# Kernel optimization log

Hardware: AMD Instinct MI355X
Metric: run time of the kernel (lower is better)

Reference implementation:

```python
import jax, jax.numpy as jnp
import numpy as np

B, C, H, W = 32, 4, 512, 512


def setup_inputs() -> dict:
    key = jax.random.key(0)
    k1, k2 = jax.random.split(key)
    out = jax.random.normal(k1, (B, C, H, W), dtype=jnp.float32)
    true_masks = jax.random.randint(k2, (B, H, W), 0, C, dtype=jnp.int32)
    return {"true_masks": true_masks, "out": out}


def reference(true_masks, out):
    n_classes = out.shape[1]
    # argmax over the class dim == torch's permute+reshape+max(dim=1)
    pred = jnp.argmax(out, axis=1).reshape(-1)          # [B*H*W]
    true = true_masks.reshape(-1)                        # [B*H*W]
    # single-pass histogram counts for all classes (replaces per-class loop)
    tp = jnp.bincount(pred, weights=(pred == true).astype(jnp.float32),
                      length=n_classes)                  # [C]
    pred_cnt = jnp.bincount(pred, length=n_classes).astype(jnp.float32)
    true_cnt = jnp.bincount(true, length=n_classes).astype(jnp.float32)
    dice = 2.0 * tp / (pred_cnt + true_cnt)              # [C]
    return dice[1:]                                      # skip background class 0
```

## Files before the change

### kernel.cpp

```cpp
#include <hip/hip_runtime.h>

constexpr int kHW       = 512 * 512;
constexpr int kC        = 4;
constexpr int kReplicas = 16;
constexpr int kLine     = 32;

constexpr int kWsInts = kReplicas * 12 * kLine;

__global__ __launch_bounds__(256)
void dice_count_kernel(const int* __restrict__ tm, const float* __restrict__ outp,
                       unsigned* __restrict__ cnt, int num_groups) {
    unsigned long long predp = 0, truep = 0, tpp = 0;

    const int stride = gridDim.x * blockDim.x;
    for (int g = blockIdx.x * blockDim.x + threadIdx.x; g < num_groups; g += stride) {
        const int b   = g >> 16;
        const int rem = (g & 0xFFFF) << 2;
        const float* base = outp + ((size_t)b * kC) * kHW + rem;
        const float4 v0 = *(const float4*)(base);
        const float4 v1 = *(const float4*)(base + kHW);
        const float4 v2 = *(const float4*)(base + 2 * kHW);
        const float4 v3 = *(const float4*)(base + 3 * kHW);
        const int4   t  = *(const int4*)(tm + (size_t)g * 4);

        #define DO_PIXEL(f, tf)                                        \
        {                                                              \
            int   pred = 0;                                            \
            float best = v0.f;                                         \
            if (v1.f > best) { best = v1.f; pred = 1; }                \
            if (v2.f > best) { best = v2.f; pred = 2; }                \
            if (v3.f > best) { best = v3.f; pred = 3; }                \
            predp += 1ull << (pred << 4);                              \
            truep += 1ull << (t.tf << 4);                              \
            if (pred == t.tf) tpp += 1ull << (pred << 4);              \
        }
        DO_PIXEL(x, x) DO_PIXEL(y, y) DO_PIXEL(z, z) DO_PIXEL(w, w)
        #undef DO_PIXEL
    }

    for (int off = 32; off > 0; off >>= 1) {
        predp += __shfl_down(predp, off);
        truep += __shfl_down(truep, off);
        tpp   += __shfl_down(tpp, off);
    }

    __shared__ unsigned long long s[3][4];
    const int lane = threadIdx.x & 63;
    const int wave = threadIdx.x >> 6;
    if (lane == 0) { s[0][wave] = predp; s[1][wave] = truep; s[2][wave] = tpp; }
    __syncthreads();

    if (threadIdx.x == 0) {
        unsigned long long P = s[0][0] + s[0][1] + s[0][2] + s[0][3];
        unsigned long long T = s[1][0] + s[1][1] + s[1][2] + s[1][3];
        unsigned long long Q = s[2][0] + s[2][1] + s[2][2] + s[2][3];
        unsigned* rep = cnt + (blockIdx.x & (kReplicas - 1)) * 12 * kLine;
        #pragma unroll
        for (int c = 0; c < 4; ++c) {
            atomicAdd(&rep[c * kLine],       (unsigned)((P >> (c * 16)) & 0xFFFF));
            atomicAdd(&rep[(4 + c) * kLine], (unsigned)((T >> (c * 16)) & 0xFFFF));
            atomicAdd(&rep[(8 + c) * kLine], (unsigned)((Q >> (c * 16)) & 0xFFFF));
        }
    }
}

__global__ void dice_final_kernel(const unsigned* __restrict__ cnt,
                                  float* __restrict__ out) {
    __shared__ float tot[12];
    if (threadIdx.x < 12) {
        unsigned sum = 0;
        #pragma unroll
        for (int r = 0; r < kReplicas; ++r)
            sum += cnt[(r * 12 + (int)threadIdx.x) * kLine];
        tot[threadIdx.x] = (float)sum;
    }
    __syncthreads();
    if (threadIdx.x >= 1 && threadIdx.x < 4) {
        const int c = (int)threadIdx.x;
        out[c - 1] = 2.0f * tot[8 + c] / (tot[c] + tot[4 + c]);
    }
}

extern "C" void kernel_launch(void* const* d_in, const int* in_sizes, int n_in,
                              void* d_out, int out_size, void* d_ws, size_t ws_size,
                              hipStream_t stream) {
    const int*   tm = (const int*)d_in[0];
    const float* op = (const float*)d_in[1];
    unsigned*   cnt = (unsigned*)d_ws;

    const int P = in_sizes[0];
    const int num_groups = P / 4;

    hipMemsetAsync(cnt, 0, kWsInts * sizeof(unsigned), stream);

    dice_count_kernel<<<1024, 256, 0, stream>>>(tm, op, cnt, num_groups);
    dice_final_kernel<<<1, 64, 0, stream>>>(cnt, (float*)d_out);
}
```

Before: 213.5 us.

## Replace atomics and memset with per-block partials and compile-time unrolled loop

Each block now writes its packed per-class partial counts to its own workspace slot instead of doing atomic adds into replicated counters. That removes the memset launch and the atomic contention. The grid doubles to 2048 blocks and the grid-stride loop becomes a fully unrolled loop with a fixed trip count, so more loads can be in flight. The final kernel reduces 2048 partials with 256 threads and shuffles. Problem sizes are now hard-coded at compile time, so the kernel no longer uses the runtime input size.

```diff
diff --git a/kernel.cpp b/kernel.cpp
--- a/kernel.cpp
+++ b/kernel.cpp
@@ -1,19 +1,25 @@
 #include <hip/hip_runtime.h>
 
-constexpr int kHW       = 512 * 512;
-constexpr int kC        = 4;
-constexpr int kReplicas = 16;
-constexpr int kLine     = 32;
+constexpr int kHW      = 512 * 512;
+constexpr int kC       = 4;
+constexpr int kB       = 32;
+constexpr int kGroups  = kB * kHW / 4;
+constexpr int kBlocks  = 2048;
+constexpr int kThreads = 256;
+constexpr int kStride  = kBlocks * kThreads;
+constexpr int kIters   = kGroups / kStride;
+static_assert(kGroups % kStride == 0, "grid must tile the group count exactly");
 
-constexpr int kWsInts = kReplicas * 12 * kLine;
 
-__global__ __launch_bounds__(256)
+__global__ __launch_bounds__(kThreads)
 void dice_count_kernel(const int* __restrict__ tm, const float* __restrict__ outp,
-                       unsigned* __restrict__ cnt, int num_groups) {
+                       unsigned long long* __restrict__ part) {
     unsigned long long predp = 0, truep = 0, tpp = 0;
+    const int tid0 = blockIdx.x * kThreads + threadIdx.x;
 
-    const int stride = gridDim.x * blockDim.x;
-    for (int g = blockIdx.x * blockDim.x + threadIdx.x; g < num_groups; g += stride) {
+    #pragma unroll
+    for (int it = 0; it < kIters; ++it) {
+        const int g   = tid0 + it * kStride;
         const int b   = g >> 16;
         const int rem = (g & 0xFFFF) << 2;
         const float* base = outp + ((size_t)b * kC) * kHW + rem;
@@ -51,33 +57,53 @@
     __syncthreads();
 
     if (threadIdx.x == 0) {
-        unsigned long long P = s[0][0] + s[0][1] + s[0][2] + s[0][3];
-        unsigned long long T = s[1][0] + s[1][1] + s[1][2] + s[1][3];
-        unsigned long long Q = s[2][0] + s[2][1] + s[2][2] + s[2][3];
-        unsigned* rep = cnt + (blockIdx.x & (kReplicas - 1)) * 12 * kLine;
-        #pragma unroll
-        for (int c = 0; c < 4; ++c) {
-            atomicAdd(&rep[c * kLine],       (unsigned)((P >> (c * 16)) & 0xFFFF));
-            atomicAdd(&rep[(4 + c) * kLine], (unsigned)((T >> (c * 16)) & 0xFFFF));
-            atomicAdd(&rep[(8 + c) * kLine], (unsigned)((Q >> (c * 16)) & 0xFFFF));
-        }
+        part[(size_t)blockIdx.x * 3 + 0] = s[0][0] + s[0][1] + s[0][2] + s[0][3];
+        part[(size_t)blockIdx.x * 3 + 1] = s[1][0] + s[1][1] + s[1][2] + s[1][3];
+        part[(size_t)blockIdx.x * 3 + 2] = s[2][0] + s[2][1] + s[2][2] + s[2][3];
     }
 }
 
-__global__ void dice_final_kernel(const unsigned* __restrict__ cnt,
-                                  float* __restrict__ out) {
-    __shared__ float tot[12];
-    if (threadIdx.x < 12) {
-        unsigned sum = 0;
+__global__ __launch_bounds__(256)
+void dice_final_kernel(const unsigned long long* __restrict__ part,
+                       float* __restrict__ out) {
+    unsigned acc[12];
+    #pragma unroll
+    for (int i = 0; i < 12; ++i) acc[i] = 0;
+
+    for (int k = threadIdx.x; k < kBlocks; k += 256) {
+        const unsigned long long P = part[(size_t)k * 3 + 0];
+        const unsigned long long T = part[(size_t)k * 3 + 1];
+        const unsigned long long Q = part[(size_t)k * 3 + 2];
         #pragma unroll
-        for (int r = 0; r < kReplicas; ++r)
-            sum += cnt[(r * 12 + (int)threadIdx.x) * kLine];
-        tot[threadIdx.x] = (float)sum;
+        for (int c = 0; c < 4; ++c) {
+            acc[c]     += (unsigned)((P >> (c * 16)) & 0xFFFF);
+            acc[4 + c] += (unsigned)((T >> (c * 16)) & 0xFFFF);
+            acc[8 + c] += (unsigned)((Q >> (c * 16)) & 0xFFFF);
+        }
+    }
+
+    #pragma unroll
+    for (int i = 0; i < 12; ++i)
+        for (int off = 32; off > 0; off >>= 1)
+            acc[i] += __shfl_down(acc[i], off);
+
+    __shared__ unsigned s[4][12];
+    const int lane = threadIdx.x & 63;
+    const int wave = threadIdx.x >> 6;
+    if (lane == 0) {
+        #pragma unroll
+        for (int i = 0; i < 12; ++i) s[wave][i] = acc[i];
     }
     __syncthreads();
-    if (threadIdx.x >= 1 && threadIdx.x < 4) {
-        const int c = (int)threadIdx.x;
-        out[c - 1] = 2.0f * tot[8 + c] / (tot[c] + tot[4 + c]);
+
+    if (threadIdx.x == 0) {
+        float tot[12];
+        #pragma unroll
+        for (int i = 0; i < 12; ++i)
+            tot[i] = (float)(s[0][i] + s[1][i] + s[2][i] + s[3][i]);
+        #pragma unroll
+        for (int c = 1; c < 4; ++c)
+            out[c - 1] = 2.0f * tot[8 + c] / (tot[c] + tot[4 + c]);
     }
 }
 
@@ -86,13 +112,8 @@
                               hipStream_t stream) {
     const int*   tm = (const int*)d_in[0];
     const float* op = (const float*)d_in[1];
-    unsigned*   cnt = (unsigned*)d_ws;
+    unsigned long long* part = (unsigned long long*)d_ws;
 
-    const int P = in_sizes[0];
-    const int num_groups = P / 4;
-
-    hipMemsetAsync(cnt, 0, kWsInts * sizeof(unsigned), stream);
-
-    dice_count_kernel<<<1024, 256, 0, stream>>>(tm, op, cnt, num_groups);
-    dice_final_kernel<<<1, 64, 0, stream>>>(cnt, (float*)d_out);
+    dice_count_kernel<<<kBlocks, kThreads, 0, stream>>>(tm, op, part);
+    dice_final_kernel<<<1, 256, 0, stream>>>(part, (float*)d_out);
 }
```

After: 211.6 us. About the same (-0.9%).
